# Optimization experiments

Hardware: AMD Instinct MI355X
Metric: run time of the kernel (lower is better)

## Reference

```python
import jax, jax.numpy as jnp
import numpy as np

N, E, C, H, DE, B = 50000, 400000, 64, 4, 16, 64
EPS = 1e-5
NEG_SLOPE = 0.2
NBLOCKS = 2


def setup_inputs() -> dict:
    key = jax.random.key(0)
    ks = jax.random.split(key, 8)
    x = jax.random.normal(ks[0], (N, C), jnp.float32)
    edge_index = jax.random.randint(ks[1], (2, E), 0, N, dtype=jnp.int64)
    edge_attr = jax.random.normal(ks[2], (E, DE), jnp.float32)
    batch = jnp.sort(jax.random.randint(ks[3], (N,), 0, B, dtype=jnp.int64))
    s = 1.0 / np.sqrt(C)
    # stacked params for the 2 blocks
    Wl = jax.random.normal(ks[4], (NBLOCKS, C, H * C), jnp.float32) * s
    Wr = jax.random.normal(ks[5], (NBLOCKS, C, H * C), jnp.float32) * s
    We = jax.random.normal(ks[6], (NBLOCKS, DE, H * C), jnp.float32) * (1.0 / np.sqrt(DE))
    att = jax.random.normal(ks[7], (NBLOCKS, H, C), jnp.float32) * s
    gat_bias = jnp.zeros((NBLOCKS, C), jnp.float32)
    gn_weight = jnp.ones((NBLOCKS, C), jnp.float32)
    gn_bias = jnp.zeros((NBLOCKS, C), jnp.float32)
    gn_mean_scale = jnp.ones((NBLOCKS, C), jnp.float32)
    return dict(x=x, edge_index=edge_index, edge_attr=edge_attr, batch=batch,
                Wl=Wl, Wr=Wr, We=We, att=att, gat_bias=gat_bias,
                gn_weight=gn_weight, gn_bias=gn_bias, gn_mean_scale=gn_mean_scale)


def _segment_mean(v, seg, num):
    s = jax.ops.segment_sum(v, seg, num_segments=num)
    cnt = jax.ops.segment_sum(jnp.ones((v.shape[0], 1), v.dtype), seg, num_segments=num)
    return s / jnp.maximum(cnt, 1.0)


def _graph_norm(x, batch, w, b, ms):
    mean = _segment_mean(x, batch, B)                 # [B, C]
    sub = x - ms * mean[batch]
    var = _segment_mean(sub * sub, batch, B)          # [B, C]
    return sub / jnp.sqrt(var[batch] + EPS) * w + b


def _gatv2(x, src, dst, ea, Wl, Wr, We, att, bias):
    # src/dst/ea already include self loops (E2 = E + N edges)
    xl = (x @ Wl).reshape(N, H, C)                    # source transform
    xr = (x @ Wr).reshape(N, H, C)                    # target transform
    ee = (ea @ We).reshape(-1, H, C)                  # [E2, H, C]
    f = jax.nn.leaky_relu(xl[src] + xr[dst] + ee, NEG_SLOPE)
    logits = jnp.einsum('ehc,hc->eh', f, att)         # [E2, H]
    m = jax.ops.segment_max(logits, dst, num_segments=N)
    a = jnp.exp(logits - m[dst])
    denom = jax.ops.segment_sum(a, dst, num_segments=N)
    alpha = a / denom[dst]                            # per-target softmax
    out = jax.ops.segment_sum(xl[src] * alpha[:, :, None], dst, num_segments=N)
    return out.mean(axis=1) + bias                    # concat=False -> head mean


def reference(x, edge_index, edge_attr, batch, Wl, Wr, We, att, gat_bias,
              gn_weight, gn_bias, gn_mean_scale):
    loop = jnp.arange(N, dtype=edge_index.dtype)
    src = jnp.concatenate([edge_index[0], loop])
    dst = jnp.concatenate([edge_index[1], loop])
    # add_self_loops with fill_value='mean'
    ea = jnp.concatenate([edge_attr,
                          jnp.broadcast_to(edge_attr.mean(axis=0), (N, DE))])
    residual = x
    for i in range(NBLOCKS):
        h = _graph_norm(x, batch, gn_weight[i], gn_bias[i], gn_mean_scale[i])
        h = jax.nn.relu(h)
        x = _gatv2(h, src, dst, ea, Wl[i], Wr[i], We[i], att[i], gat_bias[i])
    return x + residual
```

## Files before the change

kernel.cpp:

```cpp
#include <hip/hip_runtime.h>
#include <math.h>

#define NN 50000
#define EE 400000
#define ETOT 450000
#define CC 64
#define HH 4
#define DEA 16
#define NBATCH 64
#define HC 256
#define EPSV 1e-5f
#define NB 49
#define NGB 782
#define NPW 4

typedef unsigned short ushort_t;
typedef unsigned int uint_t;

__device__ __forceinline__ float4 ld4(const float* p){ return *(const float4*)p; }
__device__ __forceinline__ int rfl(int v){ return __builtin_amdgcn_readfirstlane(v); }
__device__ __forceinline__ ushort_t f2b(float f){
  uint_t u = __float_as_uint(f);
  uint_t r = (u + 0x7FFFu + ((u >> 16) & 1u)) >> 16;
  return (ushort_t)r;
}
__device__ __forceinline__ float b2f_lo(uint_t u){ return __uint_as_float(u << 16); }
__device__ __forceinline__ float b2f_hi(uint_t u){ return __uint_as_float(u & 0xFFFF0000u); }

template<int CTRL>
__device__ __forceinline__ float dpp_add(float x){
  int y = __builtin_amdgcn_update_dpp(0, __float_as_int(x), CTRL, 0xF, 0xF, true);
  return x + __int_as_float(y);
}
__device__ __forceinline__ float red16(float x){
  x = dpp_add<0xB1>(x);
  x = dpp_add<0x4E>(x);
  x = dpp_add<0x141>(x);
  x = dpp_add<0x140>(x);
  return x;
}

__global__ void k_easum(const float* __restrict__ ea, float* __restrict__ easum){
  int tid = threadIdx.x;
  int gid = blockIdx.x*256 + tid;
  int gsz = gridDim.x*256;
  float s = 0.f;
  for (long long i = gid; i < (long long)EE*DEA; i += gsz) s += ea[i];
  __shared__ float sd[256];
  sd[tid] = s; __syncthreads();
  if (tid < DEA){
    float t = 0.f;
    for (int j = tid; j < 256; j += DEA) t += sd[j];
    atomicAdd(&easum[tid], t);
  }
}

__global__ void k_hist(const int* __restrict__ dst, int* __restrict__ cnt){
  int e = blockIdx.x*256 + threadIdx.x;
  if (e < ETOT){
    int d = (e < EE) ? dst[e] : (e - EE);
    atomicAdd(&cnt[d], 1);
  }
}

__global__ __launch_bounds__(1024)
void k_scan1(const int* __restrict__ cnt, int* __restrict__ loc, int* __restrict__ bsum){
  __shared__ int wsum[16];
  int tid = threadIdx.x, lane = tid & 63, wv = tid >> 6;
  int i = blockIdx.x*1024 + tid;
  int v = (i < NN) ? cnt[i] : 0;
  int incl = v;
  #pragma unroll
  for (int off = 1; off < 64; off <<= 1){
    int t = __shfl_up(incl, off, 64);
    if (lane >= off) incl += t;
  }
  if (lane == 63) wsum[wv] = incl;
  __syncthreads();
  if (wv == 0){
    int s = (lane < 16) ? wsum[lane] : 0;
    #pragma unroll
    for (int off = 1; off < 16; off <<= 1){
      int t = __shfl_up(s, off, 64);
      if (lane >= off) s += t;
    }
    if (lane < 16) wsum[lane] = s;
  }
  __syncthreads();
  int excl = (wv ? wsum[wv-1] : 0) + incl - v;
  if (i < NN) loc[i] = excl;
  if (tid == 1023) bsum[blockIdx.x] = wsum[15];
}

__global__ void k_scan2(int* __restrict__ bsum, int* __restrict__ row_ptr){
  int lane = threadIdx.x;
  int v = (lane < NB) ? bsum[lane] : 0;
  int incl = v;
  #pragma unroll
  for (int off = 1; off < 64; off <<= 1){
    int t = __shfl_up(incl, off, 64);
    if (lane >= off) incl += t;
  }
  if (lane < NB) bsum[lane] = incl - v;
  if (lane == 63) row_ptr[NN] = incl;
}

__global__ __launch_bounds__(1024)
void k_scan3(const int* __restrict__ loc, const int* __restrict__ bsum,
             int* __restrict__ row_ptr, int* __restrict__ wp){
  int i = blockIdx.x*1024 + threadIdx.x;
  if (i < NN){
    int v = loc[i] + bsum[blockIdx.x];
    row_ptr[i] = v; wp[i] = v;
  }
}

__global__ void k_scatter(const int* __restrict__ dst, const int* __restrict__ src,
                          const float* __restrict__ ea, const float* __restrict__ easum,
                          int* __restrict__ wp, int* __restrict__ csrc,
                          float* __restrict__ eas){
  int e = blockIdx.x*256 + threadIdx.x;
  if (e >= ETOT) return;
  int d, s;
  if (e < EE){ d = dst[e]; s = src[e]; } else { d = e - EE; s = d; }
  int pos = atomicAdd(&wp[d], 1);
  csrc[pos] = s;
  float buf[16];
  if (e < EE){
    #pragma unroll
    for (int q = 0; q < 4; q++){
      float4 v = ld4(ea + (size_t)e*DEA + q*4);
      buf[q*4+0]=v.x; buf[q*4+1]=v.y; buf[q*4+2]=v.z; buf[q*4+3]=v.w;
    }
  } else {
    const float invE = 1.0f / (float)EE;
    #pragma unroll
    for (int k = 0; k < 16; k++) buf[k] = easum[k]*invE;
  }
  #pragma unroll
  for (int q = 0; q < 4; q++)
    *(float4*)(eas + (size_t)pos*DEA + q*4) =
      make_float4(buf[q*4+0], buf[q*4+1], buf[q*4+2], buf[q*4+3]);
}

__global__ void k_packw(const float* __restrict__ Wl, const float* __restrict__ Wr,
                        ushort_t* __restrict__ Wp){
  int t = blockIdx.x*256 + threadIdx.x;
  if (t >= 16384) return;
  int c4 = (t & 63) * 4;
  int k = (t >> 6) & 63;
  int mat = (t >> 12) & 1;
  int l = t >> 13;
  const float* W = (mat ? Wr : Wl) + (size_t)l*CC*HC;
  float4 w = ld4(W + (size_t)k*HC + c4);
  uint2 o;
  o.x = (uint_t)f2b(w.x) | ((uint_t)f2b(w.y) << 16);
  o.y = (uint_t)f2b(w.z) | ((uint_t)f2b(w.w) << 16);
  *(uint2*)(Wp + ((size_t)((l*2+mat)*64 + k))*HC + c4) = o;
}

__global__ __launch_bounds__(256)
void k_stats(const float* __restrict__ x, const int* __restrict__ batch,
             float* __restrict__ S, float* __restrict__ Q){
  int c = threadIdx.x & 63, g = threadIdx.x >> 6;
  int r0 = blockIdx.x*256;
  int hiR = r0 + 256; if (hiR > NN) hiR = NN;
  float s = 0.f, q = 0.f;
  int curb = -1;
  for (int n = r0 + g; n < hiR; n += 4){
    int b = batch[n];
    if (b != curb){
      if (curb >= 0){ atomicAdd(&S[curb*64+c], s); atomicAdd(&Q[curb*64+c], q); }
      curb = b; s = 0.f; q = 0.f;
    }
    float v = x[(size_t)n*CC + c];
    s += v; q += v*v;
  }
  if (curb >= 0){ atomicAdd(&S[curb*64+c], s); atomicAdd(&Q[curb*64+c], q); }
}

__device__ __forceinline__ int lowerb(const int* a, int n, int key){
  int lo = 0, hi = n;
  while (lo < hi){ int mid = (lo+hi) >> 1; if (a[mid] < key) lo = mid+1; else hi = mid; }
  return lo;
}

__global__ void k_fin(const float* __restrict__ S, const float* __restrict__ Q,
                      const int* __restrict__ batch,
                      const float* __restrict__ w, const float* __restrict__ bb,
                      const float* __restrict__ ms,
                      float* __restrict__ scale, float* __restrict__ shift){
  __shared__ float cntf;
  int b = blockIdx.x, c = threadIdx.x;
  if (c == 0){
    int lo = lowerb(batch, NN, b), hi = lowerb(batch, NN, b+1);
    cntf = fmaxf((float)(hi - lo), 1.f);
  }
  __syncthreads();
  float inv = 1.f / cntf;
  float m = S[b*64+c] * inv;
  float a = ms[c] * m;
  float var = Q[b*64+c]*inv - 2.f*a*m + a*a;
  var = fmaxf(var, 0.f);
  float rstd = rsqrtf(var + EPSV);
  float sc = rstd * w[c];
  scale[b*64+c] = sc;
  shift[b*64+c] = bb[c] - a*sc;
}

__global__ __launch_bounds__(256)
void k_gemm(const float* __restrict__ x, const int* __restrict__ batch,
            const float* __restrict__ scale, const float* __restrict__ shift,
            const ushort_t* __restrict__ WpA, const ushort_t* __restrict__ WpB,
            ushort_t* __restrict__ outA, ushort_t* __restrict__ outB){
  const ushort_t* Wp = blockIdx.z ? WpB : WpA;
  ushort_t* out = blockIdx.z ? outB : outA;
  int n0 = blockIdx.x * 64;
  __shared__ float hT[64][72];
  int tid = threadIdx.x;
  for (int t = tid; t < 1024; t += 256){
    int r = t >> 4, ch = t & 15;
    int n = n0 + r;
    float4 v = make_float4(0.f,0.f,0.f,0.f);
    if (n < NN){
      int b = batch[n];
      v = ld4(x + (size_t)n*CC + ch*4);
      float4 sc = ld4(scale + b*64 + ch*4);
      float4 sh = ld4(shift + b*64 + ch*4);
      v.x = fmaxf(v.x*sc.x + sh.x, 0.f);
      v.y = fmaxf(v.y*sc.y + sh.y, 0.f);
      v.z = fmaxf(v.z*sc.z + sh.z, 0.f);
      v.w = fmaxf(v.w*sc.w + sh.w, 0.f);
    }
    hT[ch*4+0][r] = v.x; hT[ch*4+1][r] = v.y; hT[ch*4+2][r] = v.z; hT[ch*4+3][r] = v.w;
  }
  __syncthreads();
  int c = tid & 63, rg = tid >> 6;
  int r0 = rg * 16;
  float acc[16][4];
  #pragma unroll
  for (int i = 0; i < 16; i++){ acc[i][0]=0.f; acc[i][1]=0.f; acc[i][2]=0.f; acc[i][3]=0.f; }
  #pragma unroll 4
  for (int k = 0; k < 64; k++){
    float4 a0 = *(const float4*)&hT[k][r0+0];
    float4 a1 = *(const float4*)&hT[k][r0+4];
    float4 a2 = *(const float4*)&hT[k][r0+8];
    float4 a3 = *(const float4*)&hT[k][r0+12];
    uint2 wv = *(const uint2*)(Wp + (size_t)k*HC + c*4);
    float b0 = b2f_lo(wv.x), b1 = b2f_hi(wv.x), b2 = b2f_lo(wv.y), b3 = b2f_hi(wv.y);
    const float av[16] = {a0.x,a0.y,a0.z,a0.w, a1.x,a1.y,a1.z,a1.w,
                          a2.x,a2.y,a2.z,a2.w, a3.x,a3.y,a3.z,a3.w};
    #pragma unroll
    for (int i = 0; i < 16; i++){
      acc[i][0] += av[i]*b0; acc[i][1] += av[i]*b1;
      acc[i][2] += av[i]*b2; acc[i][3] += av[i]*b3;
    }
  }
  #pragma unroll
  for (int i = 0; i < 16; i++){
    int n = n0 + r0 + i;
    if (n < NN){
      uint2 o;
      o.x = (uint_t)f2b(acc[i][0]) | ((uint_t)f2b(acc[i][1]) << 16);
      o.y = (uint_t)f2b(acc[i][2]) | ((uint_t)f2b(acc[i][3]) << 16);
      *(uint2*)(out + (size_t)n*HC + c*4) = o;
    }
  }
}

__global__ __launch_bounds__(256, 4)
void k_gat(const int* __restrict__ row_ptr, const int* __restrict__ csrc,
           const float* __restrict__ eas,
           const ushort_t* __restrict__ xlh, const ushort_t* __restrict__ xrh,
           const float* __restrict__ We, const float* __restrict__ att,
           const float* __restrict__ bias, const float* __restrict__ resid,
           float* __restrict__ out){
  int lane = threadIdx.x & 63;
  int h = lane >> 4, cg = lane & 15;
  int col = h*64 + cg*4;
  int wid = (blockIdx.x*256 + threadIdx.x) >> 6;
  int n0 = wid * NPW;
  if (n0 >= NN) return;
  int n1 = n0 + NPW; if (n1 > NN) n1 = NN;

  float wer[4][16];
  #pragma unroll
  for (int k = 0; k < 16; k++){
    float4 w = ld4(We + (size_t)k*HC + col);
    wer[0][k]=w.x; wer[1][k]=w.y; wer[2][k]=w.z; wer[3][k]=w.w;
  }
  #pragma unroll
  for (int j = 0; j < 4; j++)
    #pragma unroll
    for (int k = 0; k < 16; k++)
      asm volatile("" : "+v"(wer[j][k]));

  float4 attv = ld4(att + col);
  float4 biasv = ld4(bias + cg*4);

  for (int n = n0; n < n1; n++){
    int rr0 = rfl(row_ptr[n]), rr1 = rfl(row_ptr[n+1]);
    uint2 xrp = *(const uint2*)(xrh + (size_t)n*HC + col);
    float xr0 = b2f_lo(xrp.x), xr1 = b2f_hi(xrp.x);
    float xr2 = b2f_lo(xrp.y), xr3 = b2f_hi(xrp.y);
    float m = -3.4e38f, dsum = 0.f;
    float a0 = 0.f, a1 = 0.f, a2 = 0.f, a3 = 0.f;

    int sC = rfl(csrc[rr0]);
    uint2 xlp = *(const uint2*)(xlh + (size_t)sC*HC + col);

    for (int idx = rr0; idx < rr1; idx++){
      int idn = (idx+1 < rr1) ? idx+1 : rr0;
      int sN = rfl(csrc[idn]);
      uint2 xlq = *(const uint2*)(xlh + (size_t)sN*HC + col);

      float xl0 = b2f_lo(xlp.x), xl1 = b2f_hi(xlp.x);
      float xl2 = b2f_lo(xlp.y), xl3 = b2f_hi(xlp.y);

      const float* ep = eas + (size_t)rfl(idx)*DEA;
      float p0 = 0.f, p1 = 0.f, p2 = 0.f, p3 = 0.f;
      #pragma unroll
      for (int k = 0; k < 16; k++){
        float ek = ep[k];
        p0 += ek*wer[0][k]; p1 += ek*wer[1][k];
        p2 += ek*wer[2][k]; p3 += ek*wer[3][k];
      }
      float v0 = xl0 + xr0 + p0; v0 = (v0 > 0.f) ? v0 : 0.2f*v0;
      float v1 = xl1 + xr1 + p1; v1 = (v1 > 0.f) ? v1 : 0.2f*v1;
      float v2 = xl2 + xr2 + p2; v2 = (v2 > 0.f) ? v2 : 0.2f*v2;
      float v3 = xl3 + xr3 + p3; v3 = (v3 > 0.f) ? v3 : 0.2f*v3;
      float pl = v0*attv.x + v1*attv.y + v2*attv.z + v3*attv.w;
      pl = red16(pl);

      float mn = fmaxf(m, pl);
      float sc = __expf(m - mn);
      float wexp = __expf(pl - mn);
      dsum = dsum*sc + wexp;
      a0 = a0*sc + wexp*xl0;
      a1 = a1*sc + wexp*xl1;
      a2 = a2*sc + wexp*xl2;
      a3 = a3*sc + wexp*xl3;
      m = mn;

      xlp = xlq;
    }

    float inv = 1.0f / dsum;
    float o0 = a0*inv, o1 = a1*inv, o2 = a2*inv, o3 = a3*inv;
    #pragma unroll
    for (int off = 16; off < 64; off <<= 1){
      o0 += __shfl_xor(o0, off, 64);
      o1 += __shfl_xor(o1, off, 64);
      o2 += __shfl_xor(o2, off, 64);
      o3 += __shfl_xor(o3, off, 64);
    }
    if (lane < 16){
      float r0v = o0*0.25f + biasv.x;
      float r1v = o1*0.25f + biasv.y;
      float r2v = o2*0.25f + biasv.z;
      float r3v = o3*0.25f + biasv.w;
      if (resid){
        float4 rv = ld4(resid + (size_t)n*CC + cg*4);
        r0v += rv.x; r1v += rv.y; r2v += rv.z; r3v += rv.w;
      }
      *(float4*)(out + (size_t)n*CC + cg*4) = make_float4(r0v, r1v, r2v, r3v);
    }
  }
}

extern "C" void kernel_launch(void* const* d_in, const int* in_sizes, int n_in,
                              void* d_out, int out_size, void* d_ws, size_t ws_size,
                              hipStream_t stream) {
  const float* x     = (const float*)d_in[0];
  const int*   ei    = (const int*)d_in[1];
  const int*   src   = ei;
  const int*   dst   = ei + EE;
  const float* ea    = (const float*)d_in[2];
  const int*   batch = (const int*)d_in[3];
  const float* Wl    = (const float*)d_in[4];
  const float* Wr    = (const float*)d_in[5];
  const float* We    = (const float*)d_in[6];
  const float* att   = (const float*)d_in[7];
  const float* gb    = (const float*)d_in[8];
  const float* gw    = (const float*)d_in[9];
  const float* gnb   = (const float*)d_in[10];
  const float* gms   = (const float*)d_in[11];
  float* out = (float*)d_out;

  char* ws = (char*)d_ws;
  size_t off = 0;
  auto alloc = [&](size_t bytes) -> void* {
    void* p = ws + off; off += (bytes + 255) & ~(size_t)255; return p;
  };
  int*   cnt     = (int*)alloc(NN*sizeof(int));
  int*   loc     = (int*)alloc(NN*sizeof(int));
  int*   bsum    = (int*)alloc(64*sizeof(int));
  int*   wp      = (int*)alloc(NN*sizeof(int));
  int*   row_ptr = (int*)alloc((NN+1)*sizeof(int));
  int*   csrc    = (int*)alloc((size_t)ETOT*sizeof(int));
  float* eas     = (float*)alloc((size_t)ETOT*DEA*sizeof(float));
  float* easum   = (float*)alloc(64);
  float* statSQ  = (float*)alloc(4*4096*sizeof(float));
  float* scaleb  = (float*)alloc(4096*sizeof(float));
  float* shiftb  = (float*)alloc(4096*sizeof(float));
  ushort_t* Wp   = (ushort_t*)alloc((size_t)4*64*HC*sizeof(ushort_t));
  ushort_t* xlh  = (ushort_t*)alloc((size_t)NN*HC*sizeof(ushort_t));
  ushort_t* xrh  = (ushort_t*)alloc((size_t)NN*HC*sizeof(ushort_t));
  float* xbuf    = (float*)alloc((size_t)NN*CC*sizeof(float));
  if (off > ws_size) return;

  hipMemsetAsync(cnt, 0, NN*sizeof(int), stream);
  hipMemsetAsync(easum, 0, 64, stream);
  hipMemsetAsync(statSQ, 0, 4*4096*sizeof(float), stream);
  k_easum<<<1024, 256, 0, stream>>>(ea, easum);
  k_hist<<<(ETOT+255)/256, 256, 0, stream>>>(dst, cnt);
  k_scan1<<<NB, 1024, 0, stream>>>(cnt, loc, bsum);
  k_scan2<<<1, 64, 0, stream>>>(bsum, row_ptr);
  k_scan3<<<NB, 1024, 0, stream>>>(loc, bsum, row_ptr, wp);
  k_scatter<<<(ETOT+255)/256, 256, 0, stream>>>(dst, src, ea, easum, wp, csrc, eas);
  k_packw<<<64, 256, 0, stream>>>(Wl, Wr, Wp);

  int gatBlocks = (NN + NPW*4 - 1) / (NPW*4);
  for (int i = 0; i < 2; i++){
    const float* xin = i ? xbuf : x;
    float* S = statSQ + i*4096;
    float* Q = statSQ + 2*4096 + i*4096;
    k_stats<<<(NN+255)/256, 256, 0, stream>>>(xin, batch, S, Q);
    k_fin<<<64, 64, 0, stream>>>(S, Q, batch, gw + i*CC, gnb + i*CC, gms + i*CC, scaleb, shiftb);
    k_gemm<<<dim3(NGB, 1, 2), 256, 0, stream>>>(xin, batch, scaleb, shiftb,
                                                Wp + (size_t)(i*2+0)*64*HC,
                                                Wp + (size_t)(i*2+1)*64*HC,
                                                xlh, xrh);
    k_gat<<<gatBlocks, 256, 0, stream>>>(row_ptr, csrc, eas, xlh, xrh,
                                         We + (size_t)i*DEA*HC, att + i*HH*CC,
                                         gb + i*CC, i ? x : nullptr, i ? out : xbuf);
  }
}
```

Baseline: 452.8 us.

## Store edge attributes as fp16 pairs and use packed dot2 for edge projection

Edge attributes sorted into CSR order are now stored as packed fp16 pairs, and the We weights are kept in registers as fp16 pairs. The per-edge 16-term projection uses v_dot2 instructions, which halves the FMA count and the bytes read per edge. The next edge's attributes are prefetched one iteration ahead, and nodes per wave drop from 4 to 2 to add parallelism. The cost is lower precision (fp16 with round-toward-zero) in the edge-feature contribution.

```diff
diff --git a/kernel.cpp b/kernel.cpp
--- a/kernel.cpp
+++ b/kernel.cpp
@@ -12,10 +12,11 @@
 #define EPSV 1e-5f
 #define NB 49
 #define NGB 782
-#define NPW 4
+#define NPW 2
 
 typedef unsigned short ushort_t;
 typedef unsigned int uint_t;
+using h2t = decltype(__builtin_amdgcn_cvt_pkrtz(0.0f, 0.0f));
 
 __device__ __forceinline__ float4 ld4(const float* p){ return *(const float4*)p; }
 __device__ __forceinline__ int rfl(int v){ return __builtin_amdgcn_readfirstlane(v); }
@@ -26,6 +27,8 @@
 }
 __device__ __forceinline__ float b2f_lo(uint_t u){ return __uint_as_float(u << 16); }
 __device__ __forceinline__ float b2f_hi(uint_t u){ return __uint_as_float(u & 0xFFFF0000u); }
+__device__ __forceinline__ uint_t h2u(h2t h){ return __builtin_bit_cast(uint_t, h); }
+__device__ __forceinline__ h2t u2h(uint_t u){ return __builtin_bit_cast(h2t, u); }
 
 template<int CTRL>
 __device__ __forceinline__ float dpp_add(float x){
@@ -118,7 +121,7 @@
 __global__ void k_scatter(const int* __restrict__ dst, const int* __restrict__ src,
                           const float* __restrict__ ea, const float* __restrict__ easum,
                           int* __restrict__ wp, int* __restrict__ csrc,
-                          float* __restrict__ eas){
+                          uint_t* __restrict__ eas){
   int e = blockIdx.x*256 + threadIdx.x;
   if (e >= ETOT) return;
   int d, s;
@@ -137,10 +140,12 @@
     #pragma unroll
     for (int k = 0; k < 16; k++) buf[k] = easum[k]*invE;
   }
-  #pragma unroll
-  for (int q = 0; q < 4; q++)
-    *(float4*)(eas + (size_t)pos*DEA + q*4) =
-      make_float4(buf[q*4+0], buf[q*4+1], buf[q*4+2], buf[q*4+3]);
+  uint_t pk[8];
+  #pragma unroll
+  for (int p = 0; p < 8; p++)
+    pk[p] = h2u(__builtin_amdgcn_cvt_pkrtz(buf[2*p], buf[2*p+1]));
+  *(uint4*)(eas + (size_t)pos*8 + 0) = make_uint4(pk[0], pk[1], pk[2], pk[3]);
+  *(uint4*)(eas + (size_t)pos*8 + 4) = make_uint4(pk[4], pk[5], pk[6], pk[7]);
 }
 
 __global__ void k_packw(const float* __restrict__ Wl, const float* __restrict__ Wr,
@@ -270,7 +275,7 @@
 
 __global__ __launch_bounds__(256, 4)
 void k_gat(const int* __restrict__ row_ptr, const int* __restrict__ csrc,
-           const float* __restrict__ eas,
+           const uint_t* __restrict__ eas,
            const ushort_t* __restrict__ xlh, const ushort_t* __restrict__ xrh,
            const float* __restrict__ We, const float* __restrict__ att,
            const float* __restrict__ bias, const float* __restrict__ resid,
@@ -283,17 +288,21 @@
   if (n0 >= NN) return;
   int n1 = n0 + NPW; if (n1 > NN) n1 = NN;
 
-  float wer[4][16];
-  #pragma unroll
-  for (int k = 0; k < 16; k++){
-    float4 w = ld4(We + (size_t)k*HC + col);
-    wer[0][k]=w.x; wer[1][k]=w.y; wer[2][k]=w.z; wer[3][k]=w.w;
+  uint_t werh[4][8];
+  #pragma unroll
+  for (int p = 0; p < 8; p++){
+    float4 w0 = ld4(We + (size_t)(2*p+0)*HC + col);
+    float4 w1 = ld4(We + (size_t)(2*p+1)*HC + col);
+    werh[0][p] = h2u(__builtin_amdgcn_cvt_pkrtz(w0.x, w1.x));
+    werh[1][p] = h2u(__builtin_amdgcn_cvt_pkrtz(w0.y, w1.y));
+    werh[2][p] = h2u(__builtin_amdgcn_cvt_pkrtz(w0.z, w1.z));
+    werh[3][p] = h2u(__builtin_amdgcn_cvt_pkrtz(w0.w, w1.w));
   }
   #pragma unroll
   for (int j = 0; j < 4; j++)
     #pragma unroll
-    for (int k = 0; k < 16; k++)
-      asm volatile("" : "+v"(wer[j][k]));
+    for (int p = 0; p < 8; p++)
+      asm volatile("" : "+v"(werh[j][p]));
 
   float4 attv = ld4(att + col);
   float4 biasv = ld4(bias + cg*4);
@@ -308,22 +317,35 @@
 
     int sC = rfl(csrc[rr0]);
     uint2 xlp = *(const uint2*)(xlh + (size_t)sC*HC + col);
+    uint_t earC[8];
+    {
+      const uint_t* ep = eas + (size_t)rr0*8;
+      #pragma unroll
+      for (int p = 0; p < 8; p++) earC[p] = ep[p];
+    }
 
     for (int idx = rr0; idx < rr1; idx++){
       int idn = (idx+1 < rr1) ? idx+1 : rr0;
       int sN = rfl(csrc[idn]);
       uint2 xlq = *(const uint2*)(xlh + (size_t)sN*HC + col);
+      uint_t earN[8];
+      {
+        const uint_t* ep = eas + (size_t)rfl(idn)*8;
+        #pragma unroll
+        for (int p = 0; p < 8; p++) earN[p] = ep[p];
+      }
 
       float xl0 = b2f_lo(xlp.x), xl1 = b2f_hi(xlp.x);
       float xl2 = b2f_lo(xlp.y), xl3 = b2f_hi(xlp.y);
 
-      const float* ep = eas + (size_t)rfl(idx)*DEA;
       float p0 = 0.f, p1 = 0.f, p2 = 0.f, p3 = 0.f;
       #pragma unroll
-      for (int k = 0; k < 16; k++){
-        float ek = ep[k];
-        p0 += ek*wer[0][k]; p1 += ek*wer[1][k];
-        p2 += ek*wer[2][k]; p3 += ek*wer[3][k];
+      for (int p = 0; p < 8; p++){
+        h2t e = u2h(earC[p]);
+        p0 = __builtin_amdgcn_fdot2(e, u2h(werh[0][p]), p0, false);
+        p1 = __builtin_amdgcn_fdot2(e, u2h(werh[1][p]), p1, false);
+        p2 = __builtin_amdgcn_fdot2(e, u2h(werh[2][p]), p2, false);
+        p3 = __builtin_amdgcn_fdot2(e, u2h(werh[3][p]), p3, false);
       }
       float v0 = xl0 + xr0 + p0; v0 = (v0 > 0.f) ? v0 : 0.2f*v0;
       float v1 = xl1 + xr1 + p1; v1 = (v1 > 0.f) ? v1 : 0.2f*v1;
@@ -343,6 +365,8 @@
       m = mn;
 
       xlp = xlq;
+      #pragma unroll
+      for (int p = 0; p < 8; p++) earC[p] = earN[p];
     }
 
     float inv = 1.0f / dsum;
@@ -398,7 +422,7 @@
   int*   wp      = (int*)alloc(NN*sizeof(int));
   int*   row_ptr = (int*)alloc((NN+1)*sizeof(int));
   int*   csrc    = (int*)alloc((size_t)ETOT*sizeof(int));
-  float* eas     = (float*)alloc((size_t)ETOT*DEA*sizeof(float));
+  uint_t* eas    = (uint_t*)alloc((size_t)ETOT*8*sizeof(uint_t));
   float* easum   = (float*)alloc(64);
   float* statSQ  = (float*)alloc(4*4096*sizeof(float));
   float* scaleb  = (float*)alloc(4096*sizeof(float));
```

After: 410.9 us. 1.1x faster.
